# Optimization experiments

Measured on AMD Instinct MI355X. Metric: run time of the kernel, lower is better.

## Reference

```python
import jax, jax.numpy as jnp
import numpy as np
from jax import lax

NDIMS = 3
NUM_SCALES = 3
WINDOW_SIZE = 9
POOL_K = 3


def box_filter(x, win):
    """Separable mean (box) filter, kernel=ones/win^3, same padding. x: [N,C,D,H,W]."""
    pad = win // 2
    for ax in range(NDIMS):
        kshape = [1, 1] + [1] * NDIMS
        kshape[2 + ax] = win
        k = jnp.ones(kshape, x.dtype) / win
        padding = [(pad, pad) if i == ax else (0, 0) for i in range(NDIMS)]
        x = lax.conv_general_dilated(x, k, window_strides=(1,) * NDIMS,
                                     padding=padding,
                                     dimension_numbers=('NCDHW', 'OIDHW', 'NCDHW'))
    return x


def avg_pool3d(x, k=POOL_K, stride=2):
    """avg_pool3d with count_include_pad=False."""
    pad = k // 2
    window = (1, 1, k, k, k)
    strides = (1, 1, stride, stride, stride)
    padding = ((0, 0), (0, 0), (pad, pad), (pad, pad), (pad, pad))
    s = lax.reduce_window(x, jnp.array(0, x.dtype), lax.add, window, strides, padding)
    cnt = lax.reduce_window(jnp.ones_like(x), jnp.array(0, x.dtype), lax.add,
                            window, strides, padding)
    return s / cnt


def single_scale_ncc(Ii, Ji, win):
    mu1 = box_filter(Ii, win)
    mu2 = box_filter(Ji, win)
    sigma1_sq = box_filter(Ii * Ii, win) - mu1 * mu1
    sigma2_sq = box_filter(Ji * Ji, win) - mu2 * mu2
    sigma12 = box_filter(Ii * Ji, win) - mu1 * mu2
    eps = jnp.finfo(sigma12.dtype).eps
    cc = sigma12 * sigma12 / jnp.maximum(sigma1_sq * sigma2_sq, eps)
    return -jnp.mean(cc)


def setup_inputs() -> dict:
    key = jax.random.key(0)
    k1, k2 = jax.random.split(key)
    shape = (2, 1, 160, 192, 160)
    I = jax.random.uniform(k1, shape, dtype=jnp.float32)
    J = jax.random.uniform(k2, shape, dtype=jnp.float32)
    return {"I": I, "J": J}


def reference(I, J):
    # Multi-scale NCC: losses at windows 9/7/5 on pyramid built by stride-2 avg pooling.
    total = jnp.zeros((), I.dtype)
    for i in range(NUM_SCALES):
        # SingleScaleNCC(pred=I, target=J): Ii=target, Ji=pred (symmetric metric)
        total = total + single_scale_ncc(J, I, WINDOW_SIZE - 2 * i) / NUM_SCALES
        if i < NUM_SCALES - 1:
            I = avg_pool3d(I)
            J = avg_pool3d(J)
    return total
```

## Files before the change

### kernel.cpp

```cpp
#include <hip/hip_runtime.h>

#define NCC_EPS 1.1920929e-07f

template<int WIN>
__global__ __launch_bounds__(256)
void ncc_pad2_kernel(const float* __restrict__ Pi, const float* __restrict__ Pj,
                     int Dp, int Hp, int Wp, int Dreal, int Wreal,
                     int tilesH, int tilesW, int chunksD, int chunkLen,
                     double* __restrict__ acc)
{
    constexpr int RAD  = WIN / 2;
    constexpr int TH = 16, TW = 16;
    constexpr int WROWS = TH + 2 * RAD;
    constexpr int PSTR = 68;
    constexpr int QSTR = 16;
    constexpr int OFF  = 4 - RAD;
    constexpr int NWT  = WROWS * 4;
    constexpr int PB   = WROWS * PSTR;
    constexpr int QB   = WROWS * QSTR;
    constexpr float invV = 1.0f / (float)(WIN * WIN * WIN);

    __shared__ __align__(16) float wb0123[4][PB];
    __shared__ __align__(16) float wb4[4][QB];
    __shared__ float red[4];

    int bid = blockIdx.x;
    int tw = bid % tilesW; bid /= tilesW;
    int th = bid % tilesH; bid /= tilesH;
    int cd = bid % chunksD; bid /= chunksD;
    int b  = bid;

    const int h0 = th * TH, w0 = tw * TW;
    const int z0 = cd * chunkLen;
    const int z1 = min(z0 + chunkLen, Dreal);

    const size_t plane = (size_t)Hp * Wp;
    const float* Ib = Pi + (size_t)b * Dp * plane;
    const float* Jb = Pj + (size_t)b * Dp * plane;

    const int t  = threadIdx.x;
    const int hh = t >> 4, ww = t & 15;
    const bool valid = (w0 + ww) < Wreal;

    const int wsl  = (t >= NWT) ? 1 : 0;
    const bool wact = t < 2 * NWT;
    const int wt  = t - NWT * wsl;
    const int wr  = wt >> 2;
    const int wc4 = wt & 3;
    const size_t rowoff = (size_t)(h0 + wr) * Wp + (w0 + 4 * wc4);

    auto load_slice = [&](int zp, float (&fi)[12], float (&fj)[12]) {
        if (wact) {
            const float* rI = Ib + (size_t)zp * plane + rowoff;
            const float* rJ = Jb + (size_t)zp * plane + rowoff;
            float4 a0 = *reinterpret_cast<const float4*>(rI);
            float4 a1 = *reinterpret_cast<const float4*>(rI + 4);
            float4 a2 = *reinterpret_cast<const float4*>(rI + 8);
            float4 b0 = *reinterpret_cast<const float4*>(rJ);
            float4 b1 = *reinterpret_cast<const float4*>(rJ + 4);
            float4 b2 = *reinterpret_cast<const float4*>(rJ + 8);
            fi[0]=a0.x; fi[1]=a0.y; fi[2]=a0.z; fi[3]=a0.w;
            fi[4]=a1.x; fi[5]=a1.y; fi[6]=a1.z; fi[7]=a1.w;
            fi[8]=a2.x; fi[9]=a2.y; fi[10]=a2.z; fi[11]=a2.w;
            fj[0]=b0.x; fj[1]=b0.y; fj[2]=b0.z; fj[3]=b0.w;
            fj[4]=b1.x; fj[5]=b1.y; fj[6]=b1.z; fj[7]=b1.w;
            fj[8]=b2.x; fj[9]=b2.y; fj[10]=b2.z; fj[11]=b2.w;
        }
    };

    float ring[WIN][5];
    float rs[5];
    #pragma unroll
    for (int s = 0; s < WIN; ++s)
        #pragma unroll
        for (int c = 0; c < 5; ++c) ring[s][c] = 0.f;
    #pragma unroll
    for (int c = 0; c < 5; ++c) rs[c] = 0.f;

    float ccsum = 0.f;

    float fiC[12], fjC[12], fiN[12], fjN[12];
    const int zstart = z0 - RAD;
    const int zend   = z1 + RAD;
    load_slice(zstart + wsl + 4, fiC, fjC);

    int bufb = 0;
    for (int zb = zstart; zb < zend; zb += 2 * WIN) {
        #pragma unroll
        for (int i = 0; i < WIN; ++i) {
            const int z = zb + 2 * i;
            if (z < zend) {
                const bool haveB = (z + 1 < zend);
                const int zpn = min(z + wsl + 2 + 4, Dp - 1);
                load_slice(zpn, fiN, fjN);

                if (wact) {
                    float s0 = 0, s1 = 0, s2 = 0, s3 = 0, s4 = 0;
                    #pragma unroll
                    for (int k = 0; k < WIN; ++k) {
                        float a = fiC[OFF + k], bb = fjC[OFF + k];
                        s0 += a; s1 += bb;
                        s2 = fmaf(a, a, s2);
                        s3 = fmaf(bb, bb, s3);
                        s4 = fmaf(bb, a, s4);
                    }
                    float o0[4], o1[4], o2[4], o3[4], o4[4];
                    o0[0]=s0; o1[0]=s1; o2[0]=s2; o3[0]=s3; o4[0]=s4;
                    #pragma unroll
                    for (int m = 1; m < 4; ++m) {
                        float aL = fiC[OFF + m - 1],       bL = fjC[OFF + m - 1];
                        float aR = fiC[OFF + m - 1 + WIN], bR = fjC[OFF + m - 1 + WIN];
                        s0 += aR - aL;
                        s1 += bR - bL;
                        s2 = s2 + aR * aR - aL * aL;
                        s3 = s3 + bR * bR - bL * bL;
                        s4 = s4 + aR * bR - aL * bL;
                        o0[m]=s0; o1[m]=s1; o2[m]=s2; o3[m]=s3; o4[m]=s4;
                    }
                    float* wbW = &wb0123[bufb + wsl][0];
                    float* w4W = &wb4[bufb + wsl][0];
                    #pragma unroll
                    for (int m = 0; m < 4; ++m) {
                        *reinterpret_cast<float4*>(&wbW[wr * PSTR + 16 * wc4 + 4 * m]) =
                            make_float4(o0[m], o1[m], o2[m], o3[m]);
                    }
                    *reinterpret_cast<float4*>(&w4W[wr * QSTR + 4 * wc4]) =
                        make_float4(o4[0], o4[1], o4[2], o4[3]);
                }
                __builtin_amdgcn_sched_barrier(0);
                asm volatile("s_waitcnt lgkmcnt(0)");
                __builtin_amdgcn_s_barrier();
                __builtin_amdgcn_sched_barrier(0);
                {
                    const float* wbH = &wb0123[bufb][0];
                    const float* w4H = &wb4[bufb][0];
                    float4 a4 = make_float4(0.f, 0.f, 0.f, 0.f);
                    float nn4 = 0.f;
                    #pragma unroll
                    for (int dh = 0; dh < WIN; ++dh) {
                        float4 v = *reinterpret_cast<const float4*>(
                            &wbH[(hh + dh) * PSTR + 4 * ww]);
                        a4.x += v.x; a4.y += v.y; a4.z += v.z; a4.w += v.w;
                        nn4 += w4H[(hh + dh) * QSTR + ww];
                    }
                    rs[0] += a4.x - ring[(2 * i) % WIN][0]; ring[(2 * i) % WIN][0] = a4.x;
                    rs[1] += a4.y - ring[(2 * i) % WIN][1]; ring[(2 * i) % WIN][1] = a4.y;
                    rs[2] += a4.z - ring[(2 * i) % WIN][2]; ring[(2 * i) % WIN][2] = a4.z;
                    rs[3] += a4.w - ring[(2 * i) % WIN][3]; ring[(2 * i) % WIN][3] = a4.w;
                    rs[4] += nn4  - ring[(2 * i) % WIN][4]; ring[(2 * i) % WIN][4] = nn4;
                    const int zo = z - RAD;
                    if (valid && zo >= z0) {
                        float muI = rs[0] * invV;
                        float muJ = rs[1] * invV;
                        float sII = rs[2] * invV - muI * muI;
                        float sJJ = rs[3] * invV - muJ * muJ;
                        float s12 = rs[4] * invV - muI * muJ;
                        float cc = (s12 * s12) / fmaxf(sII * sJJ, NCC_EPS);
                        ccsum += cc;
                    }
                }
                if (haveB) {
                    const float* wbH = &wb0123[bufb + 1][0];
                    const float* w4H = &wb4[bufb + 1][0];
                    float4 a4 = make_float4(0.f, 0.f, 0.f, 0.f);
                    float nn4 = 0.f;
                    #pragma unroll
                    for (int dh = 0; dh < WIN; ++dh) {
                        float4 v = *reinterpret_cast<const float4*>(
                            &wbH[(hh + dh) * PSTR + 4 * ww]);
                        a4.x += v.x; a4.y += v.y; a4.z += v.z; a4.w += v.w;
                        nn4 += w4H[(hh + dh) * QSTR + ww];
                    }
                    rs[0] += a4.x - ring[(2 * i + 1) % WIN][0]; ring[(2 * i + 1) % WIN][0] = a4.x;
                    rs[1] += a4.y - ring[(2 * i + 1) % WIN][1]; ring[(2 * i + 1) % WIN][1] = a4.y;
                    rs[2] += a4.z - ring[(2 * i + 1) % WIN][2]; ring[(2 * i + 1) % WIN][2] = a4.z;
                    rs[3] += a4.w - ring[(2 * i + 1) % WIN][3]; ring[(2 * i + 1) % WIN][3] = a4.w;
                    rs[4] += nn4  - ring[(2 * i + 1) % WIN][4]; ring[(2 * i + 1) % WIN][4] = nn4;
                    const int zo = z + 1 - RAD;
                    if (valid && zo >= z0) {
                        float muI = rs[0] * invV;
                        float muJ = rs[1] * invV;
                        float sII = rs[2] * invV - muI * muI;
                        float sJJ = rs[3] * invV - muJ * muJ;
                        float s12 = rs[4] * invV - muI * muJ;
                        float cc = (s12 * s12) / fmaxf(sII * sJJ, NCC_EPS);
                        ccsum += cc;
                    }
                }
                #pragma unroll
                for (int e = 0; e < 12; ++e) { fiC[e] = fiN[e]; fjC[e] = fjN[e]; }
                bufb ^= 2;
            }
        }
    }

    for (int off = 32; off > 0; off >>= 1)
        ccsum += __shfl_down(ccsum, off);
    const int wid = t >> 6, lane = t & 63;
    if (lane == 0) red[wid] = ccsum;
    __syncthreads();
    if (t == 0) {
        float s = red[0] + red[1] + red[2] + red[3];
        atomicAdd(acc, (double)s);
    }
}

template<int WIN>
__global__ __launch_bounds__(256)
void ncc_pad_kernel(const float* __restrict__ Pi, const float* __restrict__ Pj,
                    int Dp, int Hp, int Wp, int Dreal, int Wreal,
                    int tilesH, int tilesW, int chunksD, int chunkLen,
                    double* __restrict__ acc)
{
    constexpr int RAD  = WIN / 2;
    constexpr int TH = 16, TW = 16;
    constexpr int WROWS = TH + 2 * RAD;
    constexpr int PSTR = 68;
    constexpr int QSTR = 16;
    constexpr int OFF  = 4 - RAD;
    constexpr int NWT  = WROWS * 4;
    constexpr float invV = 1.0f / (float)(WIN * WIN * WIN);

    __shared__ __align__(16) float wb0123[2][WROWS * PSTR];
    __shared__ __align__(16) float wb4[2][WROWS * QSTR];
    __shared__ float red[4];

    int bid = blockIdx.x;
    int tw = bid % tilesW; bid /= tilesW;
    int th = bid % tilesH; bid /= tilesH;
    int cd = bid % chunksD; bid /= chunksD;
    int b  = bid;

    const int h0 = th * TH, w0 = tw * TW;
    const int z0 = cd * chunkLen;
    const int z1 = min(z0 + chunkLen, Dreal);

    const size_t plane = (size_t)Hp * Wp;
    const float* Ib = Pi + (size_t)b * Dp * plane;
    const float* Jb = Pj + (size_t)b * Dp * plane;

    const int t  = threadIdx.x;
    const int hh = t >> 4, ww = t & 15;
    const bool valid = (w0 + ww) < Wreal;

    const int wr  = t >> 2;
    const int wc4 = t & 3;
    const bool wact = t < NWT;
    const size_t rowoff = (size_t)(h0 + wr) * Wp + (w0 + 4 * wc4);

    auto load_slice = [&](int zp, float (&fi)[12], float (&fj)[12]) {
        if (wact) {
            const float* rI = Ib + (size_t)zp * plane + rowoff;
            const float* rJ = Jb + (size_t)zp * plane + rowoff;
            float4 a0 = *reinterpret_cast<const float4*>(rI);
            float4 a1 = *reinterpret_cast<const float4*>(rI + 4);
            float4 a2 = *reinterpret_cast<const float4*>(rI + 8);
            float4 b0 = *reinterpret_cast<const float4*>(rJ);
            float4 b1 = *reinterpret_cast<const float4*>(rJ + 4);
            float4 b2 = *reinterpret_cast<const float4*>(rJ + 8);
            fi[0]=a0.x; fi[1]=a0.y; fi[2]=a0.z; fi[3]=a0.w;
            fi[4]=a1.x; fi[5]=a1.y; fi[6]=a1.z; fi[7]=a1.w;
            fi[8]=a2.x; fi[9]=a2.y; fi[10]=a2.z; fi[11]=a2.w;
            fj[0]=b0.x; fj[1]=b0.y; fj[2]=b0.z; fj[3]=b0.w;
            fj[4]=b1.x; fj[5]=b1.y; fj[6]=b1.z; fj[7]=b1.w;
            fj[8]=b2.x; fj[9]=b2.y; fj[10]=b2.z; fj[11]=b2.w;
        }
    };

    float ring[WIN][5];
    float rs[5];
    #pragma unroll
    for (int s = 0; s < WIN; ++s)
        #pragma unroll
        for (int c = 0; c < 5; ++c) ring[s][c] = 0.f;
    #pragma unroll
    for (int c = 0; c < 5; ++c) rs[c] = 0.f;

    float ccsum = 0.f;

    float fiC[12], fjC[12], fiN[12], fjN[12];
    const int zend = z1 + RAD;
    load_slice(z0 - RAD + 4, fiC, fjC);

    for (int zb = z0 - RAD; zb < zend; zb += WIN) {
        #pragma unroll
        for (int ph = 0; ph < WIN; ++ph) {
            const int z = zb + ph;
            if (z < zend) {
                const int zpn = min(z + 5, Dp - 1);
                load_slice(zpn, fiN, fjN);

                const int par = (z + 4) & 1;
                float n0, n1, n2, n3, n4;
                if (wact) {
                    float s0 = 0, s1 = 0, s2 = 0, s3 = 0, s4 = 0;
                    #pragma unroll
                    for (int k = 0; k < WIN; ++k) {
                        float a = fiC[OFF + k], bb = fjC[OFF + k];
                        s0 += a; s1 += bb;
                        s2 = fmaf(a, a, s2);
                        s3 = fmaf(bb, bb, s3);
                        s4 = fmaf(a, bb, s4);
                    }
                    float o0[4], o1[4], o2[4], o3[4], o4[4];
                    o0[0]=s0; o1[0]=s1; o2[0]=s2; o3[0]=s3; o4[0]=s4;
                    #pragma unroll
                    for (int m = 1; m < 4; ++m) {
                        float aL = fiC[OFF + m - 1],       bL = fjC[OFF + m - 1];
                        float aR = fiC[OFF + m - 1 + WIN], bR = fjC[OFF + m - 1 + WIN];
                        s0 += aR - aL;
                        s1 += bR - bL;
                        s2 = s2 + aR * aR - aL * aL;
                        s3 = s3 + bR * bR - bL * bL;
                        s4 = s4 + aR * bR - aL * bL;
                        o0[m]=s0; o1[m]=s1; o2[m]=s2; o3[m]=s3; o4[m]=s4;
                    }
                    #pragma unroll
                    for (int m = 0; m < 4; ++m) {
                        *reinterpret_cast<float4*>(&wb0123[par][wr * PSTR + 16 * wc4 + 4 * m]) =
                            make_float4(o0[m], o1[m], o2[m], o3[m]);
                    }
                    *reinterpret_cast<float4*>(&wb4[par][wr * QSTR + 4 * wc4]) =
                        make_float4(o4[0], o4[1], o4[2], o4[3]);
                }
                __builtin_amdgcn_sched_barrier(0);
                asm volatile("s_waitcnt lgkmcnt(0)");
                __builtin_amdgcn_s_barrier();
                __builtin_amdgcn_sched_barrier(0);
                {
                    float4 a4 = make_float4(0.f, 0.f, 0.f, 0.f);
                    float nn4 = 0.f;
                    #pragma unroll
                    for (int dh = 0; dh < WIN; ++dh) {
                        float4 v = *reinterpret_cast<const float4*>(
                            &wb0123[par][(hh + dh) * PSTR + 4 * ww]);
                        a4.x += v.x; a4.y += v.y; a4.z += v.z; a4.w += v.w;
                        nn4 += wb4[par][(hh + dh) * QSTR + ww];
                    }
                    n0 = a4.x; n1 = a4.y; n2 = a4.z; n3 = a4.w; n4 = nn4;
                }
                rs[0] += n0 - ring[ph][0]; ring[ph][0] = n0;
                rs[1] += n1 - ring[ph][1]; ring[ph][1] = n1;
                rs[2] += n2 - ring[ph][2]; ring[ph][2] = n2;
                rs[3] += n3 - ring[ph][3]; ring[ph][3] = n3;
                rs[4] += n4 - ring[ph][4]; ring[ph][4] = n4;

                const int zo = z - RAD;
                if (valid && zo >= z0) {
                    float muI = rs[0] * invV;
                    float muJ = rs[1] * invV;
                    float sII = rs[2] * invV - muI * muI;
                    float sJJ = rs[3] * invV - muJ * muJ;
                    float s12 = rs[4] * invV - muI * muJ;
                    float cc = (s12 * s12) / fmaxf(sII * sJJ, NCC_EPS);
                    ccsum += cc;
                }
                #pragma unroll
                for (int e = 0; e < 12; ++e) { fiC[e] = fiN[e]; fjC[e] = fjN[e]; }
            }
        }
    }

    for (int off = 32; off > 0; off >>= 1)
        ccsum += __shfl_down(ccsum, off);
    const int wid = t >> 6, lane = t & 63;
    if (lane == 0) red[wid] = ccsum;
    __syncthreads();
    if (t == 0) {
        float s = red[0] + red[1] + red[2] + red[3];
        atomicAdd(acc, (double)s);
    }
}

__global__ void pad_kernel(const float* __restrict__ inA, const float* __restrict__ inB,
                           float* __restrict__ outA, float* __restrict__ outB,
                           int D, int H, int W, int Dp, int Hp, int Wp, int nchunks)
{
    int idx = blockIdx.x * 256 + threadIdx.x;
    if (idx >= 2 * nchunks) return;
    const bool isB = idx >= nchunks;
    int k = isB ? idx - nchunks : idx;
    const float* in = isB ? inB : inA;
    float* out = isB ? outB : outA;
    const int WC = Wp / 4;
    int wc = k % WC; int tmp = k / WC;
    int hp = tmp % Hp; tmp /= Hp;
    int zp = tmp % Dp; int b = tmp / Dp;
    int z = zp - 4, h = hp - 4, w0 = 4 * wc - 4;
    float4 v = make_float4(0.f, 0.f, 0.f, 0.f);
    if (z >= 0 && z < D && h >= 0 && h < H && w0 >= 0 && w0 + 4 <= W)
        v = *reinterpret_cast<const float4*>(in + ((size_t)(b * D + z) * H + h) * W + w0);
    *reinterpret_cast<float4*>(out + ((size_t)(b * Dp + zp) * Hp + hp) * Wp + 4 * wc) = v;
}

__global__ void pool_pad_kernel(const float* __restrict__ inA, const float* __restrict__ inB,
                                float* __restrict__ outA, float* __restrict__ outB,
                                int D, int H, int W, int iDp, int iHp, int iWp,
                                int oD, int oH, int oW, int oDp, int oHp, int oWp,
                                int total)
{
    int idx0 = blockIdx.x * 256 + threadIdx.x;
    if (idx0 >= 2 * total) return;
    const bool isB = idx0 >= total;
    int idx = isB ? idx0 - total : idx0;
    const float* in = isB ? inB : inA;
    float* out = isB ? outB : outA;

    int ow = idx % oW; int tmp = idx / oW;
    int oh = tmp % oH; tmp /= oH;
    int od = tmp % oD; int b = tmp / oD;

    const size_t ip = (size_t)iHp * iWp;
    const float* ib = in + (size_t)b * iDp * ip;
    float s = 0.f;
    #pragma unroll
    for (int dd = 0; dd < 3; ++dd)
        #pragma unroll
        for (int dh = 0; dh < 3; ++dh) {
            const float* r = ib + (size_t)(2 * od + 3 + dd) * ip
                                + (size_t)(2 * oh + 3 + dh) * iWp + (2 * ow + 3);
            s += r[0] + r[1] + r[2];
        }
    int dlo = max(2 * od - 1, 0), dhi = min(2 * od + 2, D);
    int hlo = max(2 * oh - 1, 0), hhi = min(2 * oh + 2, H);
    int wlo = max(2 * ow - 1, 0), whi = min(2 * ow + 2, W);
    int cnt = (dhi - dlo) * (hhi - hlo) * (whi - wlo);
    out[((size_t)(b * oDp + od + 4) * oHp + (oh + 4)) * oWp + (ow + 4)] = s / (float)cnt;
}

template<int WIN>
__global__ __launch_bounds__(256)
void ncc_scale_kernel(const float* __restrict__ I, const float* __restrict__ J,
                      int D, int H, int W,
                      int tilesH, int tilesW, int chunksD, int chunkLen,
                      double* __restrict__ acc)
{
    constexpr int RAD  = WIN / 2;
    constexpr int TH = 16, TW = 16;
    constexpr int WROWS = TH + 2 * RAD;
    constexpr int PSTR = 68;
    constexpr int QSTR = 16;
    constexpr int OFF  = 4 - RAD;
    constexpr int NWT  = WROWS * 4;
    constexpr float invV = 1.0f / (float)(WIN * WIN * WIN);

    __shared__ __align__(16) float wb0123[2][WROWS * PSTR];
    __shared__ __align__(16) float wb4[2][WROWS * QSTR];
    __shared__ float red[4];

    int bid = blockIdx.x;
    int tw = bid % tilesW; bid /= tilesW;
    int th = bid % tilesH; bid /= tilesH;
    int cd = bid % chunksD; bid /= chunksD;
    int b  = bid;

    const int h0 = th * TH, w0 = tw * TW;
    const int z0 = cd * chunkLen;
    const int z1 = min(z0 + chunkLen, D);

    const size_t plane = (size_t)H * W;
    const float* Ib = I + (size_t)b * D * plane;
    const float* Jb = J + (size_t)b * D * plane;

    const int t  = threadIdx.x;
    const int hh = t >> 4, ww = t & 15;
    const bool valid = (h0 + hh) < H && (w0 + ww) < W;

    const int wr  = t >> 2;
    const int wc4 = t & 3;
    const bool wact = t < NWT;
    const int wbase = w0 + 4 * wc4 - 4;
    const int wghr  = h0 + wr - RAD;

    auto load_slice = [&](int z, float (&fi)[12], float (&fj)[12]) {
        const bool zok = (z >= 0) && (z < D);
        if (zok && wact && wghr >= 0 && wghr < H) {
            const float* rowI = Ib + (size_t)z * plane + (size_t)wghr * W;
            const float* rowJ = Jb + (size_t)z * plane + (size_t)wghr * W;
            if (wbase >= 0 && wbase + 12 <= W) {
                float4 a0 = *reinterpret_cast<const float4*>(rowI + wbase);
                float4 a1 = *reinterpret_cast<const float4*>(rowI + wbase + 4);
                float4 a2 = *reinterpret_cast<const float4*>(rowI + wbase + 8);
                float4 b0 = *reinterpret_cast<const float4*>(rowJ + wbase);
                float4 b1 = *reinterpret_cast<const float4*>(rowJ + wbase + 4);
                float4 b2 = *reinterpret_cast<const float4*>(rowJ + wbase + 8);
                fi[0]=a0.x; fi[1]=a0.y; fi[2]=a0.z; fi[3]=a0.w;
                fi[4]=a1.x; fi[5]=a1.y; fi[6]=a1.z; fi[7]=a1.w;
                fi[8]=a2.x; fi[9]=a2.y; fi[10]=a2.z; fi[11]=a2.w;
                fj[0]=b0.x; fj[1]=b0.y; fj[2]=b0.z; fj[3]=b0.w;
                fj[4]=b1.x; fj[5]=b1.y; fj[6]=b1.z; fj[7]=b1.w;
                fj[8]=b2.x; fj[9]=b2.y; fj[10]=b2.z; fj[11]=b2.w;
            } else {
                #pragma unroll
                for (int e = 0; e < 12; ++e) {
                    int cg = wbase + e;
                    bool ok = (cg >= 0) && (cg < W);
                    fi[e] = ok ? rowI[cg] : 0.f;
                    fj[e] = ok ? rowJ[cg] : 0.f;
                }
            }
        } else {
            #pragma unroll
            for (int e = 0; e < 12; ++e) { fi[e] = 0.f; fj[e] = 0.f; }
        }
    };

    float ring[WIN][5];
    float rs[5];
    #pragma unroll
    for (int s = 0; s < WIN; ++s)
        #pragma unroll
        for (int c = 0; c < 5; ++c) ring[s][c] = 0.f;
    #pragma unroll
    for (int c = 0; c < 5; ++c) rs[c] = 0.f;

    float ccsum = 0.f;

    float fiC[12], fjC[12], fiN[12], fjN[12];
    const int zend = z1 + RAD;
    load_slice(z0 - RAD, fiC, fjC);

    for (int zb = z0 - RAD; zb < zend; zb += WIN) {
        #pragma unroll
        for (int ph = 0; ph < WIN; ++ph) {
            const int z = zb + ph;
            if (z < zend) {
                const bool zin = (z >= 0) && (z < D);
                load_slice((z + 1 < zend) ? z + 1 : -1, fiN, fjN);
                float n0 = 0, n1 = 0, n2 = 0, n3 = 0, n4 = 0;
                if (zin) {
                    const int par = (z + 64) & 1;
                    if (wact) {
                        float s0 = 0, s1 = 0, s2 = 0, s3 = 0, s4 = 0;
                        #pragma unroll
                        for (int k = 0; k < WIN; ++k) {
                            float a = fiC[OFF + k], bb = fjC[OFF + k];
                            s0 += a; s1 += bb;
                            s2 = fmaf(a, a, s2);
                            s3 = fmaf(bb, bb, s3);
                            s4 = fmaf(a, bb, s4);
                        }
                        float o0[4], o1[4], o2[4], o3[4], o4[4];
                        o0[0]=s0; o1[0]=s1; o2[0]=s2; o3[0]=s3; o4[0]=s4;
                        #pragma unroll
                        for (int m = 1; m < 4; ++m) {
                            float aL = fiC[OFF + m - 1],       bL = fjC[OFF + m - 1];
                            float aR = fiC[OFF + m - 1 + WIN], bR = fjC[OFF + m - 1 + WIN];
                            s0 += aR - aL;
                            s1 += bR - bL;
                            s2 = s2 + aR * aR - aL * aL;
                            s3 = s3 + bR * bR - bL * bL;
                            s4 = s4 + aR * bR - aL * bL;
                            o0[m]=s0; o1[m]=s1; o2[m]=s2; o3[m]=s3; o4[m]=s4;
                        }
                        #pragma unroll
                        for (int m = 0; m < 4; ++m) {
                            *reinterpret_cast<float4*>(&wb0123[par][wr * PSTR + 16 * wc4 + 4 * m]) =
                                make_float4(o0[m], o1[m], o2[m], o3[m]);
                        }
                        *reinterpret_cast<float4*>(&wb4[par][wr * QSTR + 4 * wc4]) =
                            make_float4(o4[0], o4[1], o4[2], o4[3]);
                    }
                    __syncthreads();
                    float4 a4 = make_float4(0.f, 0.f, 0.f, 0.f);
                    #pragma unroll
                    for (int dh = 0; dh < WIN; ++dh) {
                        float4 v = *reinterpret_cast<const float4*>(
                            &wb0123[par][(hh + dh) * PSTR + 4 * ww]);
                        a4.x += v.x; a4.y += v.y; a4.z += v.z; a4.w += v.w;
                        n4 += wb4[par][(hh + dh) * QSTR + ww];
                    }
                    n0 = a4.x; n1 = a4.y; n2 = a4.z; n3 = a4.w;
                }
                rs[0] += n0 - ring[ph][0]; ring[ph][0] = n0;
                rs[1] += n1 - ring[ph][1]; ring[ph][1] = n1;
                rs[2] += n2 - ring[ph][2]; ring[ph][2] = n2;
                rs[3] += n3 - ring[ph][3]; ring[ph][3] = n3;
                rs[4] += n4 - ring[ph][4]; ring[ph][4] = n4;

                const int zo = z - RAD;
                if (valid && zo >= z0) {
                    float muI = rs[0] * invV;
                    float muJ = rs[1] * invV;
                    float sII = rs[2] * invV - muI * muI;
                    float sJJ = rs[3] * invV - muJ * muJ;
                    float s12 = rs[4] * invV - muI * muJ;
                    float cc = (s12 * s12) / fmaxf(sII * sJJ, NCC_EPS);
                    ccsum += cc;
                }
                #pragma unroll
                for (int e = 0; e < 12; ++e) { fiC[e] = fiN[e]; fjC[e] = fjN[e]; }
            }
        }
    }

    for (int off = 32; off > 0; off >>= 1)
        ccsum += __shfl_down(ccsum, off);
    const int wid = t >> 6, lane = t & 63;
    if (lane == 0) red[wid] = ccsum;
    __syncthreads();
    if (t == 0) {
        float s = red[0] + red[1] + red[2] + red[3];
        atomicAdd(acc, (double)s);
    }
}

__global__ void pool_kernel2(const float* __restrict__ inA, const float* __restrict__ inB,
                             float* __restrict__ outA, float* __restrict__ outB,
                             int D, int H, int W, int oD, int oH, int oW, int total)
{
    int idx0 = blockIdx.x * 256 + threadIdx.x;
    if (idx0 >= 2 * total) return;
    const bool isB = idx0 >= total;
    int idx = isB ? idx0 - total : idx0;
    const float* in = isB ? inB : inA;
    float* out = isB ? outB : outA;

    int ow = idx % oW; int tmp = idx / oW;
    int oh = tmp % oH; tmp /= oH;
    int od = tmp % oD; int b = tmp / oD;

    int dlo = max(2 * od - 1, 0), dhi = min(2 * od + 2, D);
    int hlo = max(2 * oh - 1, 0), hhi = min(2 * oh + 2, H);
    int wlo = max(2 * ow - 1, 0), whi = min(2 * ow + 2, W);

    const float* ib = in + (size_t)b * D * H * W;
    float s = 0.f;
    for (int d = dlo; d < dhi; ++d)
        for (int h = hlo; h < hhi; ++h)
            for (int w = wlo; w < whi; ++w)
                s += ib[((size_t)d * H + h) * W + w];
    int cnt = (dhi - dlo) * (hhi - hlo) * (whi - wlo);
    out[idx] = s / (float)cnt;
}

__global__ void finalize_kernel(const double* __restrict__ acc, float* __restrict__ out)
{
    double m = acc[0] / 9830400.0 + acc[1] / 1228800.0 + acc[2] / 153600.0;
    out[0] = (float)(-m / 3.0);
}

extern "C" void kernel_launch(void* const* d_in, const int* in_sizes, int n_in,
                              void* d_out, int out_size, void* d_ws, size_t ws_size,
                              hipStream_t stream)
{
    const float* I0 = (const float*)d_in[0];
    const float* J0 = (const float*)d_in[1];
    float* out = (float*)d_out;

    char* ws = (char*)d_ws;
    double* acc = (double*)ws;
    hipMemsetAsync(acc, 0, 3 * sizeof(double), stream);

    const size_t P0SZ = (size_t)2 * 168 * 200 * 168;
    const size_t P1SZ = (size_t)2 * 88 * 104 * 88;
    const size_t P2SZ = (size_t)2 * 48 * 56 * 56;
    const size_t need_pad = 256 + (2 * P0SZ + 2 * P1SZ + 2 * P2SZ) * sizeof(float);

    if (ws_size >= need_pad) {
        float* P0I = (float*)(ws + 256);
        float* P0J = P0I + P0SZ;
        float* P1I = P0J + P0SZ;
        float* P1J = P1I + P1SZ;
        float* P2I = P1J + P1SZ;
        float* P2J = P2I + P2SZ;

        hipMemsetAsync(P1I, 0, (2 * P1SZ + 2 * P2SZ) * sizeof(float), stream);

        {
            int nchunks = (int)(P0SZ / 4);
            int blocks = (2 * nchunks + 255) / 256;
            pad_kernel<<<blocks, 256, 0, stream>>>(I0, J0, P0I, P0J,
                                                   160, 192, 160, 168, 200, 168, nchunks);
        }
        ncc_pad2_kernel<9><<<2 * 12 * 10 * 4, 256, 0, stream>>>(
            P0I, P0J, 168, 200, 168, 160, 160, 12, 10, 4, 40, acc + 0);
        {
            int total = 2 * 80 * 96 * 80;
            int blocks = (2 * total + 255) / 256;
            pool_pad_kernel<<<blocks, 256, 0, stream>>>(P0I, P0J, P1I, P1J,
                                                        160, 192, 160, 168, 200, 168,
                                                        80, 96, 80, 88, 104, 88, total);
        }
        ncc_pad_kernel<7><<<2 * 6 * 5 * 10, 256, 0, stream>>>(
            P1I, P1J, 88, 104, 88, 80, 80, 6, 5, 10, 8, acc + 1);
        {
            int total = 2 * 40 * 48 * 40;
            int blocks = (2 * total + 255) / 256;
            pool_pad_kernel<<<blocks, 256, 0, stream>>>(P1I, P1J, P2I, P2J,
                                                        80, 96, 80, 88, 104, 88,
                                                        40, 48, 40, 48, 56, 56, total);
        }
        ncc_pad_kernel<5><<<2 * 3 * 3 * 10, 256, 0, stream>>>(
            P2I, P2J, 48, 56, 56, 40, 40, 3, 3, 10, 4, acc + 2);
    } else {
        float* I1 = (float*)(ws + 256);
        float* J1 = I1 + (size_t)2 * 80 * 96 * 80;
        float* I2 = J1 + (size_t)2 * 80 * 96 * 80;
        float* J2 = I2 + (size_t)2 * 40 * 48 * 40;

        ncc_scale_kernel<9><<<2 * 12 * 10 * 6, 256, 0, stream>>>(
            I0, J0, 160, 192, 160, 12, 10, 6, 27, acc + 0);
        {
            int total = 2 * 80 * 96 * 80;
            int blocks = (2 * total + 255) / 256;
            pool_kernel2<<<blocks, 256, 0, stream>>>(I0, J0, I1, J1,
                                                     160, 192, 160, 80, 96, 80, total);
        }
        ncc_scale_kernel<7><<<2 * 6 * 5 * 10, 256, 0, stream>>>(
            I1, J1, 80, 96, 80, 6, 5, 10, 8, acc + 1);
        {
            int total = 2 * 40 * 48 * 40;
            int blocks = (2 * total + 255) / 256;
            pool_kernel2<<<blocks, 256, 0, stream>>>(I1, J1, I2, J2,
                                                     80, 96, 80, 40, 48, 40, total);
        }
        ncc_scale_kernel<5><<<2 * 3 * 3 * 10, 256, 0, stream>>>(
            I2, J2, 40, 48, 40, 3, 3, 10, 4, acc + 2);
    }

    finalize_kernel<<<1, 1, 0, stream>>>(acc, out);
}
```

Before: 175.7 us.

## Share H-direction box sums via LDS with sliding window across threads

Adds a middle stage where half the threads compute the H-direction window sums with a sliding update and store them in new shared buffers. The final stage then reads one precomputed value instead of summing nine rows per thread. This is meant to cut redundant LDS reads and adds. In exchange it adds a second barrier per step and drops the ping-pong double buffering of the W-sum buffers.

Result: faster. 168.9 us, median of 2 (-3.9%).

```diff
diff --git a/kernel.cpp b/kernel.cpp
--- a/kernel.cpp
+++ b/kernel.cpp
@@ -4,7 +4,7 @@
 
 template<int WIN>
 __global__ __launch_bounds__(256)
-void ncc_pad2_kernel(const float* __restrict__ Pi, const float* __restrict__ Pj,
+void ncc_pad3_kernel(const float* __restrict__ Pi, const float* __restrict__ Pj,
                      int Dp, int Hp, int Wp, int Dreal, int Wreal,
                      int tilesH, int tilesW, int chunksD, int chunkLen,
                      double* __restrict__ acc)
@@ -14,14 +14,16 @@
     constexpr int WROWS = TH + 2 * RAD;
     constexpr int PSTR = 68;
     constexpr int QSTR = 16;
+    constexpr int HSTR = 68;
+    constexpr int H4STR = 16;
     constexpr int OFF  = 4 - RAD;
     constexpr int NWT  = WROWS * 4;
-    constexpr int PB   = WROWS * PSTR;
-    constexpr int QB   = WROWS * QSTR;
     constexpr float invV = 1.0f / (float)(WIN * WIN * WIN);
 
-    __shared__ __align__(16) float wb0123[4][PB];
-    __shared__ __align__(16) float wb4[4][QB];
+    __shared__ __align__(16) float wb0123[2][WROWS * PSTR];
+    __shared__ __align__(16) float wb4[2][WROWS * QSTR];
+    __shared__ __align__(16) float hw0123[2][TH * HSTR];
+    __shared__ __align__(16) float hw4[2][TH * H4STR];
     __shared__ float red[4];
 
     int bid = blockIdx.x;
@@ -48,6 +50,11 @@
     const int wr  = wt >> 2;
     const int wc4 = wt & 3;
     const size_t rowoff = (size_t)(h0 + wr) * Wp + (w0 + 4 * wc4);
+
+    const bool hact = t < 128;
+    const int hs = t >> 6;
+    const int hc = t & 15;
+    const int hg = (t >> 4) & 3;
 
     auto load_slice = [&](int zp, float (&fi)[12], float (&fj)[12]) {
         if (wact) {
@@ -84,7 +91,6 @@
     const int zend   = z1 + RAD;
     load_slice(zstart + wsl + 4, fiC, fjC);
 
-    int bufb = 0;
     for (int zb = zstart; zb < zend; zb += 2 * WIN) {
         #pragma unroll
         for (int i = 0; i < WIN; ++i) {
@@ -117,8 +123,8 @@
                         s4 = s4 + aR * bR - aL * bL;
                         o0[m]=s0; o1[m]=s1; o2[m]=s2; o3[m]=s3; o4[m]=s4;
                     }
-                    float* wbW = &wb0123[bufb + wsl][0];
-                    float* w4W = &wb4[bufb + wsl][0];
+                    float* wbW = &wb0123[wsl][0];
+                    float* w4W = &wb4[wsl][0];
                     #pragma unroll
                     for (int m = 0; m < 4; ++m) {
                         *reinterpret_cast<float4*>(&wbW[wr * PSTR + 16 * wc4 + 4 * m]) =
@@ -126,23 +132,53 @@
                     }
                     *reinterpret_cast<float4*>(&w4W[wr * QSTR + 4 * wc4]) =
                         make_float4(o4[0], o4[1], o4[2], o4[3]);
+                }
+                __builtin_amdgcn_sched_barrier(0);
+                asm volatile("s_waitcnt lgkmcnt(0)");
+                __builtin_amdgcn_s_barrier();
+                __builtin_amdgcn_sched_barrier(0);
+                if (hact) {
+                    const float* wbS = &wb0123[hs][0];
+                    const float* w4S = &wb4[hs][0];
+                    float* hwS = &hw0123[hs][0];
+                    float* h4S = &hw4[hs][0];
+                    const int r0 = 4 * hg;
+                    float4 a4 = make_float4(0.f, 0.f, 0.f, 0.f);
+                    float a1 = 0.f;
+                    float4 st4[3]; float st1[3];
+                    #pragma unroll
+                    for (int j = 0; j < WIN; ++j) {
+                        float4 v = *reinterpret_cast<const float4*>(
+                            &wbS[(r0 + j) * PSTR + 4 * hc]);
+                        float w = w4S[(r0 + j) * QSTR + hc];
+                        a4.x += v.x; a4.y += v.y; a4.z += v.z; a4.w += v.w;
+                        a1 += w;
+                        if (j < 3) { st4[j] = v; st1[j] = w; }
+                    }
+                    *reinterpret_cast<float4*>(&hwS[r0 * HSTR + 4 * hc]) = a4;
+                    h4S[r0 * H4STR + hc] = a1;
+                    #pragma unroll
+                    for (int k = 1; k < 4; ++k) {
+                        float4 vn = *reinterpret_cast<const float4*>(
+                            &wbS[(r0 + WIN - 1 + k) * PSTR + 4 * hc]);
+                        float wn = w4S[(r0 + WIN - 1 + k) * QSTR + hc];
+                        a4.x += vn.x - st4[k - 1].x;
+                        a4.y += vn.y - st4[k - 1].y;
+                        a4.z += vn.z - st4[k - 1].z;
+                        a4.w += vn.w - st4[k - 1].w;
+                        a1 += wn - st1[k - 1];
+                        *reinterpret_cast<float4*>(&hwS[(r0 + k) * HSTR + 4 * hc]) = a4;
+                        h4S[(r0 + k) * H4STR + hc] = a1;
+                    }
                 }
                 __builtin_amdgcn_sched_barrier(0);
                 asm volatile("s_waitcnt lgkmcnt(0)");
                 __builtin_amdgcn_s_barrier();
                 __builtin_amdgcn_sched_barrier(0);
                 {
-                    const float* wbH = &wb0123[bufb][0];
-                    const float* w4H = &wb4[bufb][0];
-                    float4 a4 = make_float4(0.f, 0.f, 0.f, 0.f);
-                    float nn4 = 0.f;
-                    #pragma unroll
-                    for (int dh = 0; dh < WIN; ++dh) {
-                        float4 v = *reinterpret_cast<const float4*>(
-                            &wbH[(hh + dh) * PSTR + 4 * ww]);
-                        a4.x += v.x; a4.y += v.y; a4.z += v.z; a4.w += v.w;
-                        nn4 += w4H[(hh + dh) * QSTR + ww];
-                    }
+                    float4 a4 = *reinterpret_cast<const float4*>(
+                        &hw0123[0][hh * HSTR + 4 * ww]);
+                    float nn4 = hw4[0][hh * H4STR + ww];
                     rs[0] += a4.x - ring[(2 * i) % WIN][0]; ring[(2 * i) % WIN][0] = a4.x;
                     rs[1] += a4.y - ring[(2 * i) % WIN][1]; ring[(2 * i) % WIN][1] = a4.y;
                     rs[2] += a4.z - ring[(2 * i) % WIN][2]; ring[(2 * i) % WIN][2] = a4.z;
@@ -160,17 +196,9 @@
                     }
                 }
                 if (haveB) {
-                    const float* wbH = &wb0123[bufb + 1][0];
-                    const float* w4H = &wb4[bufb + 1][0];
-                    float4 a4 = make_float4(0.f, 0.f, 0.f, 0.f);
-                    float nn4 = 0.f;
-                    #pragma unroll
-                    for (int dh = 0; dh < WIN; ++dh) {
-                        float4 v = *reinterpret_cast<const float4*>(
-                            &wbH[(hh + dh) * PSTR + 4 * ww]);
-                        a4.x += v.x; a4.y += v.y; a4.z += v.z; a4.w += v.w;
-                        nn4 += w4H[(hh + dh) * QSTR + ww];
-                    }
+                    float4 a4 = *reinterpret_cast<const float4*>(
+                        &hw0123[1][hh * HSTR + 4 * ww]);
+                    float nn4 = hw4[1][hh * H4STR + ww];
                     rs[0] += a4.x - ring[(2 * i + 1) % WIN][0]; ring[(2 * i + 1) % WIN][0] = a4.x;
                     rs[1] += a4.y - ring[(2 * i + 1) % WIN][1]; ring[(2 * i + 1) % WIN][1] = a4.y;
                     rs[2] += a4.z - ring[(2 * i + 1) % WIN][2]; ring[(2 * i + 1) % WIN][2] = a4.z;
@@ -189,7 +217,6 @@
                 }
                 #pragma unroll
                 for (int e = 0; e < 12; ++e) { fiC[e] = fiN[e]; fjC[e] = fjN[e]; }
-                bufb ^= 2;
             }
         }
     }
@@ -673,7 +700,7 @@
             pad_kernel<<<blocks, 256, 0, stream>>>(I0, J0, P0I, P0J,
                                                    160, 192, 160, 168, 200, 168, nchunks);
         }
-        ncc_pad2_kernel<9><<<2 * 12 * 10 * 4, 256, 0, stream>>>(
+        ncc_pad3_kernel<9><<<2 * 12 * 10 * 4, 256, 0, stream>>>(
             P0I, P0J, 168, 200, 168, 160, 160, 12, 10, 4, 40, acc + 0);
         {
             int total = 2 * 80 * 96 * 80;
```
